# Optimization experiments

Measured on AMD Instinct MI355X. Metric: run time of the kernel, lower is better.

Reference implementation:

```python
import jax, jax.numpy as jnp
import numpy as np

C_IN = 128      # pair channel
C_HID = 32      # per-head hidden dim
H = 4           # heads
INF = 1e9
LN_EPS = 1e-5


def setup_inputs() -> dict:
    key = jax.random.key(0)
    ks = jax.random.split(key, 8)
    B, N = 1, 256
    s = 0.02
    return {
        "x": jax.random.normal(ks[0], (B, N, N, C_IN), dtype=jnp.float32),
        "mask": jnp.ones((B, N, N), dtype=jnp.float32),
        "ln_w": jnp.ones((C_IN,), dtype=jnp.float32),
        "ln_b": jnp.zeros((C_IN,), dtype=jnp.float32),
        "w_b": jax.random.normal(ks[1], (H, C_IN), dtype=jnp.float32) * s,      # triangle-bias linear (no bias)
        "w_q": jax.random.normal(ks[2], (H * C_HID, C_IN), dtype=jnp.float32) * s,
        "w_k": jax.random.normal(ks[3], (H * C_HID, C_IN), dtype=jnp.float32) * s,
        "w_v": jax.random.normal(ks[4], (H * C_HID, C_IN), dtype=jnp.float32) * s,
        "w_g": jax.random.normal(ks[5], (H * C_HID, C_IN), dtype=jnp.float32) * s,
        "b_g": jnp.ones((H * C_HID,), dtype=jnp.float32),
        "w_o": jax.random.normal(ks[6], (C_IN, H * C_HID), dtype=jnp.float32) * s,
        "b_o": jnp.zeros((C_IN,), dtype=jnp.float32),
    }


def reference(x, mask, ln_w, ln_b, w_b, w_q, w_k, w_v, w_g, b_g, w_o, b_o):
    # starting=True -> no transpose
    # LayerNorm over channel dim
    mu = jnp.mean(x, axis=-1, keepdims=True)
    var = jnp.var(x, axis=-1, keepdims=True)
    xn = (x - mu) * jax.lax.rsqrt(var + LN_EPS) * ln_w + ln_b            # [B,I,J,C]

    # mask bias: [B, I, 1, 1, J]
    mask_bias = (INF * (mask - 1.0))[..., :, None, None, :]

    # triangle bias: linear -> [B,I,J,H] -> permute -> [B,H,I,J] -> [B,1,H,I,J]
    tri_bias = jnp.einsum("bijc,hc->bhij", xn, w_b)[:, None]

    # QKV projections, per-head: weights reshaped to [H, D, C]
    Wq = w_q.reshape(H, C_HID, C_IN)
    Wk = w_k.reshape(H, C_HID, C_IN)
    Wv = w_v.reshape(H, C_HID, C_IN)
    scale = 1.0 / np.sqrt(C_HID)
    q = jnp.einsum("bijc,hdc->bihjd", xn, Wq) * scale                    # [B,I,H,J,D]
    k = jnp.einsum("bijc,hdc->bihjd", xn, Wk)
    v = jnp.einsum("bijc,hdc->bihjd", xn, Wv)

    # attention over the J (column) axis of each row i
    a = jnp.einsum("bihqd,bihkd->bihqk", q, k) + mask_bias + tri_bias    # [B,I,H,J,J]
    a = jax.nn.softmax(a, axis=-1)
    o = jnp.einsum("bihqk,bihkd->biqhd", a, v)                           # [B,I,J,H,D]

    # sigmoid gating
    g = jax.nn.sigmoid(jnp.einsum("bijc,ec->bije", xn, w_g) + b_g)       # [B,I,J,H*D]
    o = o.reshape(*o.shape[:-2], H * C_HID) * g

    # output projection
    return jnp.einsum("bije,ce->bijc", o, w_o) + b_o                     # [B,I,J,C_in]
```

## Files before the change

### kernel.cpp

```cpp
#include <hip/hip_runtime.h>

#define N 256
#define C 128
#define H 4
#define D 32
#define NP (N*N)
#define LN_EPS 1e-5f
#define LOG2E 1.4426950408889634f

using f32x4 = __attribute__((ext_vector_type(4))) float;
using bf8   = __attribute__((ext_vector_type(8))) short;

__device__ __forceinline__ float bf2f(ushort u) {
    union { uint u; float f; } v; v.u = ((uint)u) << 16; return v.f;
}
__device__ __forceinline__ ushort f2bf(float f) {
    union { float f; uint u; } v; v.f = f;
    uint u = v.u;
    u += 0x7fffu + ((u >> 16) & 1u);
    return (ushort)(u >> 16);
}
__device__ __forceinline__ ushort f2bf_trunc(float f) {
    union { float f; uint u; } v; v.f = f;
    return (ushort)(v.u >> 16);
}

__global__ __launch_bounds__(256) void prep_weights(
    const float* __restrict__ wq, const float* __restrict__ wk,
    const float* __restrict__ wv, const float* __restrict__ wg,
    const float* __restrict__ wb, const float* __restrict__ wo,
    ushort* __restrict__ Wcat, ushort* __restrict__ Wb, ushort* __restrict__ Wo)
{
    int t = blockIdx.x * 256 + threadIdx.x;
    const float scale = 0.17677669529663689f * LOG2E;
    float v;
    if (t < 16384)       v = wq[t] * scale;
    else if (t < 32768)  v = wk[t - 16384];
    else if (t < 49152)  v = wv[t - 32768];
    else                 v = wg[t - 49152];
    Wcat[t] = f2bf(v);
    if (t < 16384) Wo[t] = f2bf(wo[t]);
    if (t < 512)   Wb[t] = f2bf(wb[t]);
}

__global__ __launch_bounds__(256) void ln_kernel(
    const float* __restrict__ x, const float* __restrict__ lnw,
    const float* __restrict__ lnb, ushort* __restrict__ xn)
{
    int wave = threadIdx.x >> 6, lane = threadIdx.x & 63;
    int p = blockIdx.x * 4 + wave;
    const float* xp = x + (size_t)p * C;
    float a0 = xp[lane], a1 = xp[lane + 64];
    float s = a0 + a1, ss = a0 * a0 + a1 * a1;
    #pragma unroll
    for (int m = 1; m < 64; m <<= 1) {
        s  += __shfl_xor(s, m, 64);
        ss += __shfl_xor(ss, m, 64);
    }
    float mean = s * (1.f / 128.f);
    float var  = ss * (1.f / 128.f) - mean * mean;
    float rstd = rsqrtf(var + LN_EPS);
    ushort* op = xn + (size_t)p * C;
    op[lane]      = f2bf((a0 - mean) * rstd * lnw[lane]      + lnb[lane]);
    op[lane + 64] = f2bf((a1 - mean) * rstd * lnw[lane + 64] + lnb[lane + 64]);
}

__global__ __launch_bounds__(256) void tri_kernel(
    const ushort* __restrict__ xn, const ushort* __restrict__ Wb,
    ushort* __restrict__ tri_p)
{
    __shared__ float wb[512];
    int t = threadIdx.x;
    wb[t]       = bf2f(Wb[t]);
    wb[t + 256] = bf2f(Wb[t + 256]);
    __syncthreads();
    int p = blockIdx.x * 256 + t;
    const ushort* xp = xn + (size_t)p * C;
    float acc0 = 0, acc1 = 0, acc2 = 0, acc3 = 0;
    #pragma unroll
    for (int c8 = 0; c8 < 16; c8++) {
        uint4 pk = ((const uint4*)xp)[c8];
        const ushort* u = (const ushort*)&pk;
        #pragma unroll
        for (int j = 0; j < 8; j++) {
            float xv = bf2f(u[j]);
            int c = c8 * 8 + j;
            acc0 += xv * wb[c];
            acc1 += xv * wb[128 + c];
            acc2 += xv * wb[256 + c];
            acc3 += xv * wb[384 + c];
        }
    }
    int q = p >> 8, k = p & 255;
    int qc = q >> 4, quad = (q >> 2) & 3, r = q & 3;
    int n = k >> 4, lrow = k & 15;
    int lane = quad * 16 + lrow;
    int v = n * 4 + r, j = v >> 3, m = v & 7;
    int base = ((qc * 8 + j) * 64 + lane) * 8 + m;
    tri_p[base]             = f2bf(acc0 * LOG2E);
    tri_p[65536 + base]     = f2bf(acc1 * LOG2E);
    tri_p[2 * 65536 + base] = f2bf(acc2 * LOG2E);
    tri_p[3 * 65536 + base] = f2bf(acc3 * LOG2E);
}

__global__ __launch_bounds__(256, 2) void proj_gemm(
    const ushort* __restrict__ xn, const ushort* __restrict__ Wcat,
    const float* __restrict__ bg,
    ushort* __restrict__ qb, ushort* __restrict__ kb,
    ushort* __restrict__ vbT, ushort* __restrict__ gate)
{
    __shared__ ushort At[128 * 128];
    __shared__ ushort Bt[128 * 128];
    int mt = blockIdx.x;
    int nt = blockIdx.y;
    int t  = threadIdx.x;

    const uint4* Ag = (const uint4*)(xn   + (size_t)mt * 128 * C);
    const uint4* Bg = (const uint4*)(Wcat + (size_t)nt * 128 * C);
    #pragma unroll
    for (int ii = 0; ii < 8; ii++) {
        int idx = t + ii * 256;
        ((uint4*)At)[idx] = Ag[idx];
        ((uint4*)Bt)[idx] = Bg[idx];
    }
    __syncthreads();

    int wave = t >> 6, lane = t & 63;
    int lrow = lane & 15, quad = lane >> 4;
    int wr = wave >> 1, wc = wave & 1;

    f32x4 acc[4][4];
    #pragma unroll
    for (int mi = 0; mi < 4; mi++)
        #pragma unroll
        for (int ni = 0; ni < 4; ni++) acc[mi][ni] = (f32x4){0.f, 0.f, 0.f, 0.f};

    #pragma unroll
    for (int ks = 0; ks < 4; ks++) {
        bf8 a[4], b[4];
        #pragma unroll
        for (int mi = 0; mi < 4; mi++)
            a[mi] = *(const bf8*)&At[(wr * 64 + mi * 16 + lrow) * 128 + ks * 32 + quad * 8];
        #pragma unroll
        for (int ni = 0; ni < 4; ni++)
            b[ni] = *(const bf8*)&Bt[(wc * 64 + ni * 16 + lrow) * 128 + ks * 32 + quad * 8];
        #pragma unroll
        for (int mi = 0; mi < 4; mi++)
            #pragma unroll
            for (int ni = 0; ni < 4; ni++)
                acc[mi][ni] = __builtin_amdgcn_mfma_f32_16x16x32_bf16(a[mi], b[ni], acc[mi][ni], 0, 0, 0);
    }

    if (nt == 2) {
        __syncthreads();
        #pragma unroll
        for (int mi = 0; mi < 4; mi++) {
            #pragma unroll
            for (int ni = 0; ni < 4; ni++) {
                int col = wc * 64 + ni * 16 + lrow;
                #pragma unroll
                for (int r = 0; r < 4; r++) {
                    int keyl = wr * 64 + mi * 16 + quad * 4 + r;
                    Bt[col * 128 + (keyl ^ (lrow << 3))] = f2bf(acc[mi][ni][r]);
                }
            }
        }
        __syncthreads();
        int i_row = mt >> 1;
        #pragma unroll
        for (int itr = 0; itr < 8; itr++) {
            int oidx = itr * 256 + t;
            int col = oidx >> 4, kc = oidx & 15;
            bf8 val = *(const bf8*)&Bt[col * 128 + ((kc * 8) ^ ((col & 15) << 3))];
            *(bf8*)&vbT[(size_t)(i_row * 128 + col) * N + (mt & 1) * 128 + kc * 8] = val;
        }
    } else {
        ushort* dst = (nt == 0) ? qb : (nt == 1) ? kb : gate;
        bool gated = (nt == 3);
        #pragma unroll
        for (int mi = 0; mi < 4; mi++) {
            #pragma unroll
            for (int ni = 0; ni < 4; ni++) {
                int col = wc * 64 + ni * 16 + lrow;
                #pragma unroll
                for (int r = 0; r < 4; r++) {
                    int row = mt * 128 + wr * 64 + mi * 16 + quad * 4 + r;
                    float v = acc[mi][ni][r];
                    if (gated) v = 1.f / (1.f + __expf(-(v + bg[col])));
                    dst[(size_t)row * C + col] = f2bf(v);
                }
            }
        }
    }
}

__global__ __launch_bounds__(512, 4) void attn_kernel(
    const ushort* __restrict__ qb, const ushort* __restrict__ kb,
    const ushort* __restrict__ vbT, const ushort* __restrict__ tri_p,
    const float* __restrict__ mask, ushort* __restrict__ ob)
{
    __shared__ ushort Kf[8192];
    __shared__ ushort Vf[8192];
    __shared__ ushort Pf[8][2048];

    int i  = blockIdx.x;
    int h  = blockIdx.y;
    int t  = threadIdx.x;
    int wave = t >> 6, lane = t & 63;
    int lrow = lane & 15, quad = lane >> 4;

    {
        const ushort* kt = kb + (size_t)(i * N) * C + h * D;
        #pragma unroll
        for (int it = 0; it < 2; it++) {
            int idx = it * 512 + t;
            int key = idx >> 2, d0 = (idx & 3) * 8;
            bf8 kv = *(const bf8*)(kt + (size_t)key * C + d0);
            int c = (idx >> 6) * 64 + (idx & 3) * 16 + ((idx >> 2) & 15);
            *(bf8*)&Kf[c * 8] = kv;
        }
    }
    {
        const ushort* vt = vbT + (size_t)((i * H + h) * D) * N;
        #pragma unroll
        for (int it = 0; it < 2; it++) {
            int idx = it * 512 + t;
            bf8 vv = *(const bf8*)(vt + idx * 8);
            int c = (idx >> 9) * 512 + ((idx >> 2) & 7) * 64 + (idx & 3) * 16 + ((idx >> 5) & 15);
            c ^= (c >> 6) & 7;
            *(bf8*)&Vf[c * 8] = vv;
        }
    }
    float mb[16];
    #pragma unroll
    for (int n = 0; n < 16; n++)
        mb[n] = (1e9f * LOG2E) * (mask[i * N + n * 16 + lrow] - 1.0f);
    __syncthreads();

    ushort* Pw = &Pf[wave][0];
    const ushort* trih = tri_p + (size_t)h * 65536;
    int pq = quad * 32 + (lrow & 7);
    int l3 = (lrow >> 3) & 1;

    #pragma unroll 1
    for (int cc = 0; cc < 2; cc++) {
        int qc = wave * 2 + cc;
        bf8 aq = *(const bf8*)(qb + (size_t)(i * N + qc * 16 + lrow) * C + h * D + quad * 8);
        float sum[4] = {0.f, 0.f, 0.f, 0.f};
        f32x4 o[2];
        o[0] = (f32x4){0.f, 0.f, 0.f, 0.f};
        o[1] = (f32x4){0.f, 0.f, 0.f, 0.f};

        #pragma unroll
        for (int half = 0; half < 2; half++) {
            f32x4 s8[8];
            #pragma unroll
            for (int n8 = 0; n8 < 8; n8++) {
                bf8 kf = *(const bf8*)&Kf[((half * 8 + n8) * 64 + lane) * 8];
                s8[n8] = __builtin_amdgcn_mfma_f32_16x16x32_bf16(
                    aq, kf, (f32x4){0.f, 0.f, 0.f, 0.f}, 0, 0, 0);
            }
            const ushort* tp = trih + ((size_t)(qc * 8 + half * 4) * 64 + lane) * 8;
            bf8 tf[4];
            #pragma unroll
            for (int jj = 0; jj < 4; jj++)
                tf[jj] = *(const bf8*)(tp + jj * 512);

            #pragma unroll
            for (int n8 = 0; n8 < 8; n8++) {
                int pa = (n8 >> 1) * 512 + (((n8 << 1) + l3) & 3) * 128 + pq;
                #pragma unroll
                for (int r = 0; r < 4; r++) {
                    float tb = bf2f(((const ushort*)&tf[n8 >> 1])[((n8 & 1) << 2) + r]);
                    float e  = exp2f(s8[n8][r] + tb + mb[half * 8 + n8]);
                    sum[r]  += e;
                    Pw[pa + r * 8] = f2bf_trunc(e);
                }
            }
            __asm__ volatile("s_waitcnt lgkmcnt(0)" ::: "memory");

            #pragma unroll
            for (int ks = 0; ks < 4; ks++) {
                bf8 ap = *(const bf8*)&Pw[(ks * 64 + lane) * 8];
                int ksg = half * 4 + ks;
                #pragma unroll
                for (int nv = 0; nv < 2; nv++) {
                    int c = nv * 512 + ksg * 64 + (lane ^ (ksg & 7));
                    bf8 bv = *(const bf8*)&Vf[c * 8];
                    o[nv] = __builtin_amdgcn_mfma_f32_16x16x32_bf16(ap, bv, o[nv], 0, 0, 0);
                }
            }
        }
        #pragma unroll
        for (int r = 0; r < 4; r++) {
            float s = sum[r];
            s += __shfl_xor(s, 1, 64);
            s += __shfl_xor(s, 2, 64);
            s += __shfl_xor(s, 4, 64);
            s += __shfl_xor(s, 8, 64);
            sum[r] = 1.f / s;
        }
        #pragma unroll
        for (int nv = 0; nv < 2; nv++) {
            int d = nv * 16 + lrow;
            #pragma unroll
            for (int r = 0; r < 4; r++) {
                int qg = qc * 16 + quad * 4 + r;
                ob[(size_t)(i * N + qg) * C + h * D + d] = f2bf(o[nv][r] * sum[r]);
            }
        }
    }
}

__global__ __launch_bounds__(256, 2) void out_gemm(
    const ushort* __restrict__ ob, const ushort* __restrict__ gate,
    const ushort* __restrict__ Wo, const float* __restrict__ bo,
    float* __restrict__ out)
{
    __shared__ ushort At[128 * 128];
    __shared__ ushort Bt[128 * 128];
    int mt = blockIdx.x;
    int t  = threadIdx.x;

    const uint4* Og = (const uint4*)(ob   + (size_t)mt * 128 * C);
    const uint4* Gg = (const uint4*)(gate + (size_t)mt * 128 * C);
    const uint4* Bg = (const uint4*)Wo;
    #pragma unroll
    for (int ii = 0; ii < 8; ii++) {
        int idx = t + ii * 256;
        uint4 o4 = Og[idx], g4 = Gg[idx], r4;
        const ushort* os = (const ushort*)&o4;
        const ushort* gs = (const ushort*)&g4;
        ushort* rs = (ushort*)&r4;
        #pragma unroll
        for (int j = 0; j < 8; j++) rs[j] = f2bf(bf2f(os[j]) * bf2f(gs[j]));
        ((uint4*)At)[idx] = r4;
        ((uint4*)Bt)[idx] = Bg[idx];
    }
    __syncthreads();

    int wave = t >> 6, lane = t & 63;
    int lrow = lane & 15, quad = lane >> 4;
    int wr = wave >> 1, wc = wave & 1;

    f32x4 acc[4][4];
    #pragma unroll
    for (int mi = 0; mi < 4; mi++)
        #pragma unroll
        for (int ni = 0; ni < 4; ni++) acc[mi][ni] = (f32x4){0.f, 0.f, 0.f, 0.f};

    #pragma unroll
    for (int ks = 0; ks < 4; ks++) {
        bf8 a[4], b[4];
        #pragma unroll
        for (int mi = 0; mi < 4; mi++)
            a[mi] = *(const bf8*)&At[(wr * 64 + mi * 16 + lrow) * 128 + ks * 32 + quad * 8];
        #pragma unroll
        for (int ni = 0; ni < 4; ni++)
            b[ni] = *(const bf8*)&Bt[(wc * 64 + ni * 16 + lrow) * 128 + ks * 32 + quad * 8];
        #pragma unroll
        for (int mi = 0; mi < 4; mi++)
            #pragma unroll
            for (int ni = 0; ni < 4; ni++)
                acc[mi][ni] = __builtin_amdgcn_mfma_f32_16x16x32_bf16(a[mi], b[ni], acc[mi][ni], 0, 0, 0);
    }

    #pragma unroll
    for (int mi = 0; mi < 4; mi++) {
        #pragma unroll
        for (int ni = 0; ni < 4; ni++) {
            int col = wc * 64 + ni * 16 + lrow;
            float bias = bo[col];
            #pragma unroll
            for (int r = 0; r < 4; r++) {
                int row = mt * 128 + wr * 64 + mi * 16 + quad * 4 + r;
                out[(size_t)row * C + col] = acc[mi][ni][r] + bias;
            }
        }
    }
}

extern "C" void kernel_launch(void* const* d_in, const int* in_sizes, int n_in,
                              void* d_out, int out_size, void* d_ws, size_t ws_size,
                              hipStream_t stream)
{
    const float* x    = (const float*)d_in[0];
    const float* mask = (const float*)d_in[1];
    const float* lnw  = (const float*)d_in[2];
    const float* lnb  = (const float*)d_in[3];
    const float* wb   = (const float*)d_in[4];
    const float* wq   = (const float*)d_in[5];
    const float* wk   = (const float*)d_in[6];
    const float* wv   = (const float*)d_in[7];
    const float* wg   = (const float*)d_in[8];
    const float* bg   = (const float*)d_in[9];
    const float* wo   = (const float*)d_in[10];
    const float* bo   = (const float*)d_in[11];
    float* out = (float*)d_out;

    uintptr_t w = (uintptr_t)d_ws;
    ushort* xn    = (ushort*)w; w += (size_t)NP * C * 2;
    ushort* qb    = (ushort*)w; w += (size_t)NP * C * 2;
    ushort* kb    = (ushort*)w; w += (size_t)NP * C * 2;
    ushort* vbT   = (ushort*)w; w += (size_t)NP * C * 2;
    ushort* gate  = (ushort*)w; w += (size_t)NP * C * 2;
    ushort* ob    = (ushort*)w; w += (size_t)NP * C * 2;
    ushort* tri_p = (ushort*)w; w += (size_t)H * NP * 2;
    ushort* Wcat  = (ushort*)w; w += 512 * 128 * 2;
    ushort* Wb    = (ushort*)w; w += 512 * 2;
    ushort* Wo    = (ushort*)w; w += 128 * 128 * 2;

    prep_weights<<<256, 256, 0, stream>>>(wq, wk, wv, wg, wb, wo, Wcat, Wb, Wo);
    ln_kernel<<<NP / 4, 256, 0, stream>>>(x, lnw, lnb, xn);
    tri_kernel<<<NP / 256, 256, 0, stream>>>(xn, Wb, tri_p);
    proj_gemm<<<dim3(NP / 128, 4), 256, 0, stream>>>(xn, Wcat, bg, qb, kb, vbT, gate);
    attn_kernel<<<dim3(N, H), 512, 0, stream>>>(qb, kb, vbT, tri_p, mask, ob);
    out_gemm<<<NP / 128, 256, 0, stream>>>(ob, gate, Wo, bo, out);
}
```

Measured before the change: 196.5 us.

## Fuse LN, QKV/gate projections, attention and output GEMM into one per-row kernel

Replaces the chain of LN, projection GEMM, attention and output GEMM kernels with a single per-row kernel. Each block recomputes LayerNorm for its row into shared memory, projects Q/K/V/gate per head with MFMA, runs attention, and accumulates the gated output projection across heads in registers. The triangle bias is folded into a combined LN+tri kernel. This removes the large bf16 intermediate round-trips through global memory (xn, q, k, vT, gate, o) and several launches. In exchange the grid drops to 256 blocks with heavy shared memory and register use, so the GPU runs at lower occupancy, and LN is computed twice.

```diff
diff --git a/kernel.cpp b/kernel.cpp
--- a/kernel.cpp
+++ b/kernel.cpp
@@ -28,8 +28,8 @@
 __global__ __launch_bounds__(256) void prep_weights(
     const float* __restrict__ wq, const float* __restrict__ wk,
     const float* __restrict__ wv, const float* __restrict__ wg,
-    const float* __restrict__ wb, const float* __restrict__ wo,
-    ushort* __restrict__ Wcat, ushort* __restrict__ Wb, ushort* __restrict__ Wo)
+    const float* __restrict__ wo,
+    ushort* __restrict__ Wcat, ushort* __restrict__ Wo)
 {
     int t = blockIdx.x * 256 + threadIdx.x;
     const float scale = 0.17677669529663689f * LOG2E;
@@ -40,12 +40,12 @@
     else                 v = wg[t - 49152];
     Wcat[t] = f2bf(v);
     if (t < 16384) Wo[t] = f2bf(wo[t]);
-    if (t < 512)   Wb[t] = f2bf(wb[t]);
-}
-
-__global__ __launch_bounds__(256) void ln_kernel(
+}
+
+__global__ __launch_bounds__(256) void ln_tri_kernel(
     const float* __restrict__ x, const float* __restrict__ lnw,
-    const float* __restrict__ lnb, ushort* __restrict__ xn)
+    const float* __restrict__ lnb, const float* __restrict__ wb,
+    ushort* __restrict__ tri_p)
 {
     int wave = threadIdx.x >> 6, lane = threadIdx.x & 63;
     int p = blockIdx.x * 4 + wave;
@@ -60,175 +60,71 @@
     float mean = s * (1.f / 128.f);
     float var  = ss * (1.f / 128.f) - mean * mean;
     float rstd = rsqrtf(var + LN_EPS);
-    ushort* op = xn + (size_t)p * C;
-    op[lane]      = f2bf((a0 - mean) * rstd * lnw[lane]      + lnb[lane]);
-    op[lane + 64] = f2bf((a1 - mean) * rstd * lnw[lane + 64] + lnb[lane + 64]);
-}
-
-__global__ __launch_bounds__(256) void tri_kernel(
-    const ushort* __restrict__ xn, const ushort* __restrict__ Wb,
-    ushort* __restrict__ tri_p)
+    float v0 = (a0 - mean) * rstd * lnw[lane]      + lnb[lane];
+    float v1 = (a1 - mean) * rstd * lnw[lane + 64] + lnb[lane + 64];
+
+    float t[H];
+    #pragma unroll
+    for (int h = 0; h < H; h++)
+        t[h] = v0 * wb[h * C + lane] + v1 * wb[h * C + 64 + lane];
+    #pragma unroll
+    for (int m = 1; m < 64; m <<= 1) {
+        #pragma unroll
+        for (int h = 0; h < H; h++) t[h] += __shfl_xor(t[h], m, 64);
+    }
+    if (lane == 0) {
+        int q = p >> 8, k = p & 255;
+        int qc = q >> 4, quad = (q >> 2) & 3, r = q & 3;
+        int n = k >> 4, lrow = k & 15;
+        int ln2 = quad * 16 + lrow;
+        int v = n * 4 + r, j = v >> 3, m = v & 7;
+        int base = ((qc * 8 + j) * 64 + ln2) * 8 + m;
+        #pragma unroll
+        for (int h = 0; h < H; h++)
+            tri_p[h * 65536 + base] = f2bf(t[h] * LOG2E);
+    }
+}
+
+__global__ __launch_bounds__(512, 2) void fused_row(
+    const float* __restrict__ x, const float* __restrict__ lnw,
+    const float* __restrict__ lnb, const ushort* __restrict__ Wcat,
+    const float* __restrict__ bg, const ushort* __restrict__ Wo,
+    const float* __restrict__ bo, const ushort* __restrict__ tri_p,
+    const float* __restrict__ mask, float* __restrict__ out)
 {
-    __shared__ float wb[512];
-    int t = threadIdx.x;
-    wb[t]       = bf2f(Wb[t]);
-    wb[t + 256] = bf2f(Wb[t + 256]);
-    __syncthreads();
-    int p = blockIdx.x * 256 + t;
-    const ushort* xp = xn + (size_t)p * C;
-    float acc0 = 0, acc1 = 0, acc2 = 0, acc3 = 0;
-    #pragma unroll
-    for (int c8 = 0; c8 < 16; c8++) {
-        uint4 pk = ((const uint4*)xp)[c8];
-        const ushort* u = (const ushort*)&pk;
-        #pragma unroll
-        for (int j = 0; j < 8; j++) {
-            float xv = bf2f(u[j]);
-            int c = c8 * 8 + j;
-            acc0 += xv * wb[c];
-            acc1 += xv * wb[128 + c];
-            acc2 += xv * wb[256 + c];
-            acc3 += xv * wb[384 + c];
-        }
-    }
-    int q = p >> 8, k = p & 255;
-    int qc = q >> 4, quad = (q >> 2) & 3, r = q & 3;
-    int n = k >> 4, lrow = k & 15;
-    int lane = quad * 16 + lrow;
-    int v = n * 4 + r, j = v >> 3, m = v & 7;
-    int base = ((qc * 8 + j) * 64 + lane) * 8 + m;
-    tri_p[base]             = f2bf(acc0 * LOG2E);
-    tri_p[65536 + base]     = f2bf(acc1 * LOG2E);
-    tri_p[2 * 65536 + base] = f2bf(acc2 * LOG2E);
-    tri_p[3 * 65536 + base] = f2bf(acc3 * LOG2E);
-}
-
-__global__ __launch_bounds__(256, 2) void proj_gemm(
-    const ushort* __restrict__ xn, const ushort* __restrict__ Wcat,
-    const float* __restrict__ bg,
-    ushort* __restrict__ qb, ushort* __restrict__ kb,
-    ushort* __restrict__ vbT, ushort* __restrict__ gate)
-{
-    __shared__ ushort At[128 * 128];
-    __shared__ ushort Bt[128 * 128];
-    int mt = blockIdx.x;
-    int nt = blockIdx.y;
-    int t  = threadIdx.x;
-
-    const uint4* Ag = (const uint4*)(xn   + (size_t)mt * 128 * C);
-    const uint4* Bg = (const uint4*)(Wcat + (size_t)nt * 128 * C);
-    #pragma unroll
-    for (int ii = 0; ii < 8; ii++) {
-        int idx = t + ii * 256;
-        ((uint4*)At)[idx] = Ag[idx];
-        ((uint4*)Bt)[idx] = Bg[idx];
-    }
-    __syncthreads();
-
-    int wave = t >> 6, lane = t & 63;
-    int lrow = lane & 15, quad = lane >> 4;
-    int wr = wave >> 1, wc = wave & 1;
-
-    f32x4 acc[4][4];
-    #pragma unroll
-    for (int mi = 0; mi < 4; mi++)
-        #pragma unroll
-        for (int ni = 0; ni < 4; ni++) acc[mi][ni] = (f32x4){0.f, 0.f, 0.f, 0.f};
-
-    #pragma unroll
-    for (int ks = 0; ks < 4; ks++) {
-        bf8 a[4], b[4];
-        #pragma unroll
-        for (int mi = 0; mi < 4; mi++)
-            a[mi] = *(const bf8*)&At[(wr * 64 + mi * 16 + lrow) * 128 + ks * 32 + quad * 8];
-        #pragma unroll
-        for (int ni = 0; ni < 4; ni++)
-            b[ni] = *(const bf8*)&Bt[(wc * 64 + ni * 16 + lrow) * 128 + ks * 32 + quad * 8];
-        #pragma unroll
-        for (int mi = 0; mi < 4; mi++)
-            #pragma unroll
-            for (int ni = 0; ni < 4; ni++)
-                acc[mi][ni] = __builtin_amdgcn_mfma_f32_16x16x32_bf16(a[mi], b[ni], acc[mi][ni], 0, 0, 0);
-    }
-
-    if (nt == 2) {
-        __syncthreads();
-        #pragma unroll
-        for (int mi = 0; mi < 4; mi++) {
-            #pragma unroll
-            for (int ni = 0; ni < 4; ni++) {
-                int col = wc * 64 + ni * 16 + lrow;
-                #pragma unroll
-                for (int r = 0; r < 4; r++) {
-                    int keyl = wr * 64 + mi * 16 + quad * 4 + r;
-                    Bt[col * 128 + (keyl ^ (lrow << 3))] = f2bf(acc[mi][ni][r]);
-                }
-            }
-        }
-        __syncthreads();
-        int i_row = mt >> 1;
-        #pragma unroll
-        for (int itr = 0; itr < 8; itr++) {
-            int oidx = itr * 256 + t;
-            int col = oidx >> 4, kc = oidx & 15;
-            bf8 val = *(const bf8*)&Bt[col * 128 + ((kc * 8) ^ ((col & 15) << 3))];
-            *(bf8*)&vbT[(size_t)(i_row * 128 + col) * N + (mt & 1) * 128 + kc * 8] = val;
-        }
-    } else {
-        ushort* dst = (nt == 0) ? qb : (nt == 1) ? kb : gate;
-        bool gated = (nt == 3);
-        #pragma unroll
-        for (int mi = 0; mi < 4; mi++) {
-            #pragma unroll
-            for (int ni = 0; ni < 4; ni++) {
-                int col = wc * 64 + ni * 16 + lrow;
-                #pragma unroll
-                for (int r = 0; r < 4; r++) {
-                    int row = mt * 128 + wr * 64 + mi * 16 + quad * 4 + r;
-                    float v = acc[mi][ni][r];
-                    if (gated) v = 1.f / (1.f + __expf(-(v + bg[col])));
-                    dst[(size_t)row * C + col] = f2bf(v);
-                }
-            }
-        }
-    }
-}
-
-__global__ __launch_bounds__(512, 4) void attn_kernel(
-    const ushort* __restrict__ qb, const ushort* __restrict__ kb,
-    const ushort* __restrict__ vbT, const ushort* __restrict__ tri_p,
-    const float* __restrict__ mask, ushort* __restrict__ ob)
-{
+    __shared__ ushort Xs[128 * 256];
+    __shared__ ushort Qf[8192];
     __shared__ ushort Kf[8192];
     __shared__ ushort Vf[8192];
     __shared__ ushort Pf[8][2048];
 
-    int i  = blockIdx.x;
-    int h  = blockIdx.y;
-    int t  = threadIdx.x;
+    int i    = blockIdx.x;
+    int t    = threadIdx.x;
     int wave = t >> 6, lane = t & 63;
     int lrow = lane & 15, quad = lane >> 4;
 
     {
-        const ushort* kt = kb + (size_t)(i * N) * C + h * D;
-        #pragma unroll
-        for (int it = 0; it < 2; it++) {
-            int idx = it * 512 + t;
-            int key = idx >> 2, d0 = (idx & 3) * 8;
-            bf8 kv = *(const bf8*)(kt + (size_t)key * C + d0);
-            int c = (idx >> 6) * 64 + (idx & 3) * 16 + ((idx >> 2) & 15);
-            *(bf8*)&Kf[c * 8] = kv;
-        }
-    }
-    {
-        const ushort* vt = vbT + (size_t)((i * H + h) * D) * N;
-        #pragma unroll
-        for (int it = 0; it < 2; it++) {
-            int idx = it * 512 + t;
-            bf8 vv = *(const bf8*)(vt + idx * 8);
-            int c = (idx >> 9) * 512 + ((idx >> 2) & 7) * 64 + (idx & 3) * 16 + ((idx >> 5) & 15);
-            c ^= (c >> 6) & 7;
-            *(bf8*)&Vf[c * 8] = vv;
+        const float* xp = x + ((size_t)(i * N) + wave * 32) * C;
+        float lw0 = lnw[lane], lw1 = lnw[lane + 64];
+        float lb0 = lnb[lane], lb1 = lnb[lane + 64];
+        #pragma unroll 4
+        for (int jj = 0; jj < 32; jj++) {
+            float a0 = xp[jj * C + lane], a1 = xp[jj * C + 64 + lane];
+            float s = a0 + a1, ss = a0 * a0 + a1 * a1;
+            #pragma unroll
+            for (int m = 1; m < 64; m <<= 1) {
+                s  += __shfl_xor(s, m, 64);
+                ss += __shfl_xor(ss, m, 64);
+            }
+            float mean = s * (1.f / 128.f);
+            float var  = ss * (1.f / 128.f) - mean * mean;
+            float rstd = rsqrtf(var + LN_EPS);
+            int p = wave * 32 + jj;
+            int c80 = lane >> 3, c81 = 8 + (lane >> 3);
+            Xs[(p * 16 + (c80 ^ (p & 7))) * 8 + (lane & 7)] =
+                f2bf((a0 - mean) * rstd * lw0 + lb0);
+            Xs[(p * 16 + (c81 ^ (p & 7))) * 8 + (lane & 7)] =
+                f2bf((a1 - mean) * rstd * lw1 + lb1);
         }
     }
     float mb[16];
@@ -237,144 +133,217 @@
         mb[n] = (1e9f * LOG2E) * (mask[i * N + n * 16 + lrow] - 1.0f);
     __syncthreads();
 
+    bf8 xf[2][4];
+    #pragma unroll
+    for (int tt = 0; tt < 2; tt++)
+        #pragma unroll
+        for (int ks = 0; ks < 4; ks++) {
+            int pr = (wave * 2 + tt) * 16 + lrow;
+            xf[tt][ks] = *(const bf8*)&Xs[(pr * 16 + ((ks * 4 + quad) ^ (pr & 7))) * 8];
+        }
+
+    f32x4 outacc[2][8];
+    #pragma unroll
+    for (int cc = 0; cc < 2; cc++)
+        #pragma unroll
+        for (int n8 = 0; n8 < 8; n8++) outacc[cc][n8] = (f32x4){0.f, 0.f, 0.f, 0.f};
+
     ushort* Pw = &Pf[wave][0];
-    const ushort* trih = tri_p + (size_t)h * 65536;
     int pq = quad * 32 + (lrow & 7);
     int l3 = (lrow >> 3) & 1;
 
     #pragma unroll 1
+    for (int h = 0; h < H; h++) {
+        const ushort* trih = tri_p + (size_t)h * 65536;
+        {
+            const ushort* WqB = Wcat + (size_t)(h * D) * C;
+            const ushort* WkB = Wcat + (size_t)(128 + h * D) * C;
+            bf8 aQ[2][4], aK[2][4];
+            #pragma unroll
+            for (int mm = 0; mm < 2; mm++)
+                #pragma unroll
+                for (int ks = 0; ks < 4; ks++) {
+                    aQ[mm][ks] = *(const bf8*)(WqB + (size_t)(mm * 16 + lrow) * C + ks * 32 + quad * 8);
+                    aK[mm][ks] = *(const bf8*)(WkB + (size_t)(mm * 16 + lrow) * C + ks * 32 + quad * 8);
+                }
+            #pragma unroll
+            for (int tt = 0; tt < 2; tt++) {
+                int n = wave * 2 + tt;
+                f32x4 accQ[2], accK[2];
+                #pragma unroll
+                for (int mm = 0; mm < 2; mm++) {
+                    accQ[mm] = (f32x4){0.f, 0.f, 0.f, 0.f};
+                    accK[mm] = (f32x4){0.f, 0.f, 0.f, 0.f};
+                }
+                #pragma unroll
+                for (int ks = 0; ks < 4; ks++)
+                    #pragma unroll
+                    for (int mm = 0; mm < 2; mm++) {
+                        accQ[mm] = __builtin_amdgcn_mfma_f32_16x16x32_bf16(aQ[mm][ks], xf[tt][ks], accQ[mm], 0, 0, 0);
+                        accK[mm] = __builtin_amdgcn_mfma_f32_16x16x32_bf16(aK[mm][ks], xf[tt][ks], accK[mm], 0, 0, 0);
+                    }
+                #pragma unroll
+                for (int mm = 0; mm < 2; mm++) {
+                    int addr = n * 512 + (mm * 2 + (quad >> 1)) * 128 + lrow * 8 + (quad & 1) * 4;
+                    ushort4 pk;
+                    pk.x = f2bf(accQ[mm][0]); pk.y = f2bf(accQ[mm][1]);
+                    pk.z = f2bf(accQ[mm][2]); pk.w = f2bf(accQ[mm][3]);
+                    *(ushort4*)&Qf[addr] = pk;
+                    pk.x = f2bf(accK[mm][0]); pk.y = f2bf(accK[mm][1]);
+                    pk.z = f2bf(accK[mm][2]); pk.w = f2bf(accK[mm][3]);
+                    *(ushort4*)&Kf[addr] = pk;
+                }
+            }
+            const ushort* WvB = Wcat + (size_t)(256 + h * D) * C;
+            bf8 bV[2][4];
+            #pragma unroll
+            for (int nn = 0; nn < 2; nn++)
+                #pragma unroll
+                for (int ks = 0; ks < 4; ks++)
+                    bV[nn][ks] = *(const bf8*)(WvB + (size_t)(nn * 16 + lrow) * C + ks * 32 + quad * 8);
+            #pragma unroll
+            for (int tt = 0; tt < 2; tt++) {
+                int m = wave * 2 + tt;
+                f32x4 accV[2];
+                accV[0] = (f32x4){0.f, 0.f, 0.f, 0.f};
+                accV[1] = (f32x4){0.f, 0.f, 0.f, 0.f};
+                #pragma unroll
+                for (int ks = 0; ks < 4; ks++)
+                    #pragma unroll
+                    for (int nn = 0; nn < 2; nn++)
+                        accV[nn] = __builtin_amdgcn_mfma_f32_16x16x32_bf16(xf[tt][ks], bV[nn][ks], accV[nn], 0, 0, 0);
+                #pragma unroll
+                for (int nn = 0; nn < 2; nn++) {
+                    int d = nn * 16 + lrow;
+                    int addr = (d * 32 + ((m * 2 + (quad >> 1)) ^ (lrow & 7))) * 8 + (quad & 1) * 4;
+                    ushort4 pk;
+                    pk.x = f2bf(accV[nn][0]); pk.y = f2bf(accV[nn][1]);
+                    pk.z = f2bf(accV[nn][2]); pk.w = f2bf(accV[nn][3]);
+                    *(ushort4*)&Vf[addr] = pk;
+                }
+            }
+        }
+        __syncthreads();
+
+        f32x4 o[2][2];
+        float inv[2][4];
+        #pragma unroll
+        for (int cc = 0; cc < 2; cc++) {
+            int qc = wave * 2 + cc;
+            bf8 aq = *(const bf8*)&Qf[qc * 512 + quad * 128 + lrow * 8];
+            float sum[4] = {0.f, 0.f, 0.f, 0.f};
+            o[cc][0] = (f32x4){0.f, 0.f, 0.f, 0.f};
+            o[cc][1] = (f32x4){0.f, 0.f, 0.f, 0.f};
+
+            #pragma unroll
+            for (int hf = 0; hf < 2; hf++) {
+                f32x4 s8[8];
+                #pragma unroll
+                for (int n8 = 0; n8 < 8; n8++) {
+                    bf8 kf = *(const bf8*)&Kf[(hf * 8 + n8) * 512 + quad * 128 + lrow * 8];
+                    s8[n8] = __builtin_amdgcn_mfma_f32_16x16x32_bf16(
+                        aq, kf, (f32x4){0.f, 0.f, 0.f, 0.f}, 0, 0, 0);
+                }
+                const ushort* tp = trih + ((size_t)(qc * 8 + hf * 4) * 64 + lane) * 8;
+                bf8 tf[4];
+                #pragma unroll
+                for (int jj = 0; jj < 4; jj++)
+                    tf[jj] = *(const bf8*)(tp + jj * 512);
+
+                #pragma unroll
+                for (int n8 = 0; n8 < 8; n8++) {
+                    int pa = (n8 >> 1) * 512 + (((n8 << 1) + l3) & 3) * 128 + pq;
+                    #pragma unroll
+                    for (int r = 0; r < 4; r++) {
+                        float tb = bf2f(((const ushort*)&tf[n8 >> 1])[((n8 & 1) << 2) + r]);
+                        float e  = exp2f(s8[n8][r] + tb + mb[hf * 8 + n8]);
+                        sum[r]  += e;
+                        Pw[pa + r * 8] = f2bf_trunc(e);
+                    }
+                }
+                __asm__ volatile("s_waitcnt lgkmcnt(0)" ::: "memory");
+
+                #pragma unroll
+                for (int ks = 0; ks < 4; ks++) {
+                    bf8 ap = *(const bf8*)&Pw[(ks * 64 + lane) * 8];
+                    int ksg = hf * 4 + ks;
+                    #pragma unroll
+                    for (int nv = 0; nv < 2; nv++) {
+                        bf8 bv = *(const bf8*)&Vf[((nv * 16 + lrow) * 32 + ((ksg * 4 + quad) ^ (lrow & 7))) * 8];
+                        o[cc][nv] = __builtin_amdgcn_mfma_f32_16x16x32_bf16(ap, bv, o[cc][nv], 0, 0, 0);
+                    }
+                }
+            }
+            #pragma unroll
+            for (int r = 0; r < 4; r++) {
+                float s = sum[r];
+                s += __shfl_xor(s, 1, 64);
+                s += __shfl_xor(s, 2, 64);
+                s += __shfl_xor(s, 4, 64);
+                s += __shfl_xor(s, 8, 64);
+                inv[cc][r] = 1.f / s;
+            }
+        }
+
+        {
+            const ushort* WgB = Wcat + (size_t)(384 + h * D) * C;
+            bf8 gW[2][4];
+            float bgv[2];
+            #pragma unroll
+            for (int nn = 0; nn < 2; nn++) {
+                bgv[nn] = bg[h * D + nn * 16 + lrow];
+                #pragma unroll
+                for (int ks = 0; ks < 4; ks++)
+                    gW[nn][ks] = *(const bf8*)(WgB + (size_t)(nn * 16 + lrow) * C + ks * 32 + quad * 8);
+            }
+            #pragma unroll
+            for (int cc = 0; cc < 2; cc++) {
+                f32x4 gacc[2];
+                gacc[0] = (f32x4){0.f, 0.f, 0.f, 0.f};
+                gacc[1] = (f32x4){0.f, 0.f, 0.f, 0.f};
+                #pragma unroll
+                for (int ks = 0; ks < 4; ks++)
+                    #pragma unroll
+                    for (int nn = 0; nn < 2; nn++)
+                        gacc[nn] = __builtin_amdgcn_mfma_f32_16x16x32_bf16(xf[cc][ks], gW[nn][ks], gacc[nn], 0, 0, 0);
+                #pragma unroll
+                for (int nv = 0; nv < 2; nv++) {
+                    #pragma unroll
+                    for (int r = 0; r < 4; r++) {
+                        float g  = 1.f / (1.f + __expf(-(gacc[nv][r] + bgv[nv])));
+                        float og = o[cc][nv][r] * inv[cc][r] * g;
+                        Pw[cc * 512 + (nv * 2 + (lrow >> 3)) * 128 + (quad * 4 + r) * 8 + (lrow & 7)]
+                            = f2bf(og);
+                    }
+                }
+            }
+            __asm__ volatile("s_waitcnt lgkmcnt(0)" ::: "memory");
+
+            bf8 woB[8];
+            #pragma unroll
+            for (int n8 = 0; n8 < 8; n8++)
+                woB[n8] = *(const bf8*)(Wo + (size_t)(n8 * 16 + lrow) * 128 + h * D + quad * 8);
+            #pragma unroll
+            for (int cc = 0; cc < 2; cc++) {
+                bf8 ag = *(const bf8*)&Pw[cc * 512 + quad * 128 + lrow * 8];
+                #pragma unroll
+                for (int n8 = 0; n8 < 8; n8++)
+                    outacc[cc][n8] = __builtin_amdgcn_mfma_f32_16x16x32_bf16(ag, woB[n8], outacc[cc][n8], 0, 0, 0);
+            }
+        }
+        __syncthreads();
+    }
+
+    #pragma unroll
     for (int cc = 0; cc < 2; cc++) {
-        int qc = wave * 2 + cc;
-        bf8 aq = *(const bf8*)(qb + (size_t)(i * N + qc * 16 + lrow) * C + h * D + quad * 8);
-        float sum[4] = {0.f, 0.f, 0.f, 0.f};
-        f32x4 o[2];
-        o[0] = (f32x4){0.f, 0.f, 0.f, 0.f};
-        o[1] = (f32x4){0.f, 0.f, 0.f, 0.f};
-
-        #pragma unroll
-        for (int half = 0; half < 2; half++) {
-            f32x4 s8[8];
-            #pragma unroll
-            for (int n8 = 0; n8 < 8; n8++) {
-                bf8 kf = *(const bf8*)&Kf[((half * 8 + n8) * 64 + lane) * 8];
-                s8[n8] = __builtin_amdgcn_mfma_f32_16x16x32_bf16(
-                    aq, kf, (f32x4){0.f, 0.f, 0.f, 0.f}, 0, 0, 0);
-            }
-            const ushort* tp = trih + ((size_t)(qc * 8 + half * 4) * 64 + lane) * 8;
-            bf8 tf[4];
-            #pragma unroll
-            for (int jj = 0; jj < 4; jj++)
-                tf[jj] = *(const bf8*)(tp + jj * 512);
-
-            #pragma unroll
-            for (int n8 = 0; n8 < 8; n8++) {
-                int pa = (n8 >> 1) * 512 + (((n8 << 1) + l3) & 3) * 128 + pq;
-                #pragma unroll
-                for (int r = 0; r < 4; r++) {
-                    float tb = bf2f(((const ushort*)&tf[n8 >> 1])[((n8 & 1) << 2) + r]);
-                    float e  = exp2f(s8[n8][r] + tb + mb[half * 8 + n8]);
-                    sum[r]  += e;
-                    Pw[pa + r * 8] = f2bf_trunc(e);
-                }
-            }
-            __asm__ volatile("s_waitcnt lgkmcnt(0)" ::: "memory");
-
-            #pragma unroll
-            for (int ks = 0; ks < 4; ks++) {
-                bf8 ap = *(const bf8*)&Pw[(ks * 64 + lane) * 8];
-                int ksg = half * 4 + ks;
-                #pragma unroll
-                for (int nv = 0; nv < 2; nv++) {
-                    int c = nv * 512 + ksg * 64 + (lane ^ (ksg & 7));
-                    bf8 bv = *(const bf8*)&Vf[c * 8];
-                    o[nv] = __builtin_amdgcn_mfma_f32_16x16x32_bf16(ap, bv, o[nv], 0, 0, 0);
-                }
-            }
-        }
-        #pragma unroll
-        for (int r = 0; r < 4; r++) {
-            float s = sum[r];
-            s += __shfl_xor(s, 1, 64);
-            s += __shfl_xor(s, 2, 64);
-            s += __shfl_xor(s, 4, 64);
-            s += __shfl_xor(s, 8, 64);
-            sum[r] = 1.f / s;
-        }
-        #pragma unroll
-        for (int nv = 0; nv < 2; nv++) {
-            int d = nv * 16 + lrow;
+        #pragma unroll
+        for (int n8 = 0; n8 < 8; n8++) {
+            int col = n8 * 16 + lrow;
+            float bias = bo[col];
             #pragma unroll
             for (int r = 0; r < 4; r++) {
-                int qg = qc * 16 + quad * 4 + r;
-                ob[(size_t)(i * N + qg) * C + h * D + d] = f2bf(o[nv][r] * sum[r]);
-            }
-        }
-    }
-}
-
-__global__ __launch_bounds__(256, 2) void out_gemm(
-    const ushort* __restrict__ ob, const ushort* __restrict__ gate,
-    const ushort* __restrict__ Wo, const float* __restrict__ bo,
-    float* __restrict__ out)
-{
-    __shared__ ushort At[128 * 128];
-    __shared__ ushort Bt[128 * 128];
-    int mt = blockIdx.x;
-    int t  = threadIdx.x;
-
-    const uint4* Og = (const uint4*)(ob   + (size_t)mt * 128 * C);
-    const uint4* Gg = (const uint4*)(gate + (size_t)mt * 128 * C);
-    const uint4* Bg = (const uint4*)Wo;
-    #pragma unroll
-    for (int ii = 0; ii < 8; ii++) {
-        int idx = t + ii * 256;
-        uint4 o4 = Og[idx], g4 = Gg[idx], r4;
-        const ushort* os = (const ushort*)&o4;
-        const ushort* gs = (const ushort*)&g4;
-        ushort* rs = (ushort*)&r4;
-        #pragma unroll
-        for (int j = 0; j < 8; j++) rs[j] = f2bf(bf2f(os[j]) * bf2f(gs[j]));
-        ((uint4*)At)[idx] = r4;
-        ((uint4*)Bt)[idx] = Bg[idx];
-    }
-    __syncthreads();
-
-    int wave = t >> 6, lane = t & 63;
-    int lrow = lane & 15, quad = lane >> 4;
-    int wr = wave >> 1, wc = wave & 1;
-
-    f32x4 acc[4][4];
-    #pragma unroll
-    for (int mi = 0; mi < 4; mi++)
-        #pragma unroll
-        for (int ni = 0; ni < 4; ni++) acc[mi][ni] = (f32x4){0.f, 0.f, 0.f, 0.f};
-
-    #pragma unroll
-    for (int ks = 0; ks < 4; ks++) {
-        bf8 a[4], b[4];
-        #pragma unroll
-        for (int mi = 0; mi < 4; mi++)
-            a[mi] = *(const bf8*)&At[(wr * 64 + mi * 16 + lrow) * 128 + ks * 32 + quad * 8];
-        #pragma unroll
-        for (int ni = 0; ni < 4; ni++)
-            b[ni] = *(const bf8*)&Bt[(wc * 64 + ni * 16 + lrow) * 128 + ks * 32 + quad * 8];
-        #pragma unroll
-        for (int mi = 0; mi < 4; mi++)
-            #pragma unroll
-            for (int ni = 0; ni < 4; ni++)
-                acc[mi][ni] = __builtin_amdgcn_mfma_f32_16x16x32_bf16(a[mi], b[ni], acc[mi][ni], 0, 0, 0);
-    }
-
-    #pragma unroll
-    for (int mi = 0; mi < 4; mi++) {
-        #pragma unroll
-        for (int ni = 0; ni < 4; ni++) {
-            int col = wc * 64 + ni * 16 + lrow;
-            float bias = bo[col];
-            #pragma unroll
-            for (int r = 0; r < 4; r++) {
-                int row = mt * 128 + wr * 64 + mi * 16 + quad * 4 + r;
-                out[(size_t)row * C + col] = acc[mi][ni][r] + bias;
+                int q = (wave * 2 + cc) * 16 + quad * 4 + r;
+                out[((size_t)(i * N + q)) * C + col] = outacc[cc][n8][r] + bias;
             }
         }
     }
@@ -399,21 +368,11 @@
     float* out = (float*)d_out;
 
     uintptr_t w = (uintptr_t)d_ws;
-    ushort* xn    = (ushort*)w; w += (size_t)NP * C * 2;
-    ushort* qb    = (ushort*)w; w += (size_t)NP * C * 2;
-    ushort* kb    = (ushort*)w; w += (size_t)NP * C * 2;
-    ushort* vbT   = (ushort*)w; w += (size_t)NP * C * 2;
-    ushort* gate  = (ushort*)w; w += (size_t)NP * C * 2;
-    ushort* ob    = (ushort*)w; w += (size_t)NP * C * 2;
     ushort* tri_p = (ushort*)w; w += (size_t)H * NP * 2;
     ushort* Wcat  = (ushort*)w; w += 512 * 128 * 2;
-    ushort* Wb    = (ushort*)w; w += 512 * 2;
     ushort* Wo    = (ushort*)w; w += 128 * 128 * 2;
 
-    prep_weights<<<256, 256, 0, stream>>>(wq, wk, wv, wg, wb, wo, Wcat, Wb, Wo);
-    ln_kernel<<<NP / 4, 256, 0, stream>>>(x, lnw, lnb, xn);
-    tri_kernel<<<NP / 256, 256, 0, stream>>>(xn, Wb, tri_p);
-    proj_gemm<<<dim3(NP / 128, 4), 256, 0, stream>>>(xn, Wcat, bg, qb, kb, vbT, gate);
-    attn_kernel<<<dim3(N, H), 512, 0, stream>>>(qb, kb, vbT, tri_p, mask, ob);
-    out_gemm<<<NP / 128, 256, 0, stream>>>(ob, gate, Wo, bo, out);
-}
+    prep_weights<<<256, 256, 0, stream>>>(wq, wk, wv, wg, wo, Wcat, Wo);
+    ln_tri_kernel<<<NP / 4, 256, 0, stream>>>(x, lnw, lnb, wb, tri_p);
+    fused_row<<<N, 512, 0, stream>>>(x, lnw, lnb, Wcat, bg, Wo, bo, tri_p, mask, out);
+}
```

Measured after the change: 207.5 us. 1.06x slower.
